# Optimization experiments

Measured on AMD Instinct MI355X. Metric: run time of the kernel, lower is better.

Reference implementation:

```python
import jax, jax.numpy as jnp
import numpy as np

B, S, H, KVH, D, MD = 4, 4096, 2, 1, 2, 5  # batch, seq, heads, kv heads, head_dim, model_dim
EPS, SCALE = 1e-6, 16.0


def _rmsnorm(t):
    # RMSNormNoWeight with scale=16.0 over last dim
    var = jnp.mean(t * t, axis=-1, keepdims=True)
    return SCALE * t * jax.lax.rsqrt(var + EPS)


def _rope(t, cos, sin):
    # t: (B, S, h, D); cos/sin: (S, D//2). Complex multiply on interleaved pairs.
    tr, ti = t[..., 0::2], t[..., 1::2]
    c = cos[None, :, None, :]
    s = sin[None, :, None, :]
    out_r = tr * c - ti * s
    out_i = tr * s + ti * c
    return jnp.stack([out_r, out_i], axis=-1).reshape(t.shape)


def setup_inputs() -> dict:
    key = jax.random.key(0)
    ks = jax.random.split(key, 9)
    return {
        "x": jax.random.normal(ks[0], (B, S, MD), jnp.float32),
        "freqs": jax.random.normal(ks[1], (S, D // 2), jnp.float32),
        "shared_qk_v": jax.random.normal(ks[2], (MD,), jnp.float32),
        "shared_v_v": jax.random.normal(ks[3], (MD,), jnp.float32),
        "shared_o_v": jax.random.normal(ks[4], (H * D,), jnp.float32),
        "shared_vproj_u": jax.random.normal(ks[5], (KVH * D,), jnp.float32),
        "q_u": jax.random.normal(ks[6], (H * D,), jnp.float32),
        "k_u": jax.random.normal(ks[7], (KVH * D,), jnp.float32),
        "o_u": jax.random.normal(ks[8], (MD,), jnp.float32),
    }


def reference(x, freqs, shared_qk_v, shared_v_v, shared_o_v, shared_vproj_u, q_u, k_u, o_u):
    b, s = x.shape[0], x.shape[1]
    # rank-1 projections: (x . v) outer u
    s_qk = jnp.sum(x * shared_qk_v, axis=-1, keepdims=True)  # (B,S,1) shared by q and k
    q = (s_qk * q_u).reshape(b, s, H, D)
    k = (s_qk * k_u).reshape(b, s, KVH, D)
    s_v = jnp.sum(x * shared_v_v, axis=-1, keepdims=True)
    v = (s_v * shared_vproj_u).reshape(b, s, KVH, D)
    # qk-norm + rotary
    q = _rmsnorm(q)
    k = _rmsnorm(k)
    cos, sin = jnp.cos(freqs), jnp.sin(freqs)
    q = _rope(q, cos, sin)
    k = _rope(k, cos, sin)
    # (B,h,S,D)
    q = q.transpose(0, 2, 1, 3)
    k = k.transpose(0, 2, 1, 3)
    v = v.transpose(0, 2, 1, 3)
    # GQA repeat kv heads
    k = jnp.repeat(k, H // KVH, axis=1)
    v = jnp.repeat(v, H // KVH, axis=1)
    scores = jnp.einsum('bhqd,bhkd->bhqk', q, k) / jnp.sqrt(jnp.float32(D))
    probs = jax.nn.softmax(scores, axis=-1)
    out = jnp.einsum('bhqk,bhkd->bhqd', probs, v)
    out = out.transpose(0, 2, 1, 3).reshape(b, s, H * D)
    # rank-1 output projection
    s_o = jnp.sum(out * shared_o_v, axis=-1, keepdims=True)
    return s_o * o_u  # (B,S,MODEL_DIM)
```

## Files before the change

### kernel.cpp

```cpp
#include <hip/hip_runtime.h>
#include <math.h>


#define BQ 4
#define SQ 4096
#define MDQ 5
#define EPSQ 1e-6f
#define SCALEQ 16.0f
#define L2E 1.4426950408889634f
#define ISQ2 0.70710678118654752f

__device__ __forceinline__ float fast_exp2(float x) {
#if __has_builtin(__builtin_amdgcn_exp2f)
    return __builtin_amdgcn_exp2f(x);
#else
    return __expf(x * 0.6931471805599453f);
#endif
}

__global__ __launch_bounds__(256)
void ca_prep(const float* __restrict__ x, const float* __restrict__ freqs,
             const float* __restrict__ qk_v, const float* __restrict__ v_v,
             const float* __restrict__ k_u, float4* __restrict__ pqc)
{
    const int idx = blockIdx.x * 256 + threadIdx.x;
    const int j   = idx & (SQ - 1);

    const float w0 = k_u[0], w1 = k_u[1];
    const float mk = 0.5f * (w0 * w0 + w1 * w1);

    const float qk0 = qk_v[0], qk1 = qk_v[1], qk2 = qk_v[2], qk3 = qk_v[3], qk4 = qk_v[4];
    const float vv0 = v_v[0],  vv1 = v_v[1],  vv2 = v_v[2],  vv3 = v_v[3],  vv4 = v_v[4];

    const float* xr = x + (size_t)idx * MDQ;
    const float x0 = xr[0], x1 = xr[1], x2 = xr[2], x3 = xr[3], x4 = xr[4];
    const float a  = x0*qk0 + x1*qk1 + x2*qk2 + x3*qk3 + x4*qk4;
    const float sv = x0*vv0 + x1*vv1 + x2*vv2 + x3*vv3 + x4*vv4;

    float sj, cj;
    __sincosf(freqs[j], &sj, &cj);
    const float mu = SCALEQ * a * rsqrtf(a * a * mk + EPSQ);
    pqc[idx] = make_float4(mu * cj, mu * sj, sv, 0.0f);
}

#define BLOCK 256
#define ROWS 16
#define SPLIT 16
#define JSUB (SQ / SPLIT)
#define TILES (SQ / ROWS)

__global__ __launch_bounds__(BLOCK)
void ca_main(const float* __restrict__ x,
             const float* __restrict__ freqs,
             const float* __restrict__ qk_v,
             const float* __restrict__ o_v,
             const float* __restrict__ vproj_u,
             const float* __restrict__ q_u,
             const float* __restrict__ k_u,
             const float* __restrict__ o_u,
             const float4* __restrict__ pqc,
             float* __restrict__ out)
{
    __shared__ float4 sRed[ROWS][SPLIT];

    const int tid  = threadIdx.x;
    const int bx   = blockIdx.x;
    const int b    = bx / TILES;
    const int tile = bx % TILES;
    const int row  = tid & (ROWS - 1);
    const int sp   = tid / ROWS;
    const int i    = tile * ROWS + row;

    const float w0 = k_u[0], w1 = k_u[1];
    const float mk  = 0.5f * (w0 * w0 + w1 * w1);
    const float Mmu = SCALEQ * rsqrtf(mk);

    const float qk0 = qk_v[0], qk1 = qk_v[1], qk2 = qk_v[2], qk3 = qk_v[3], qk4 = qk_v[4];
    const float u00 = q_u[0], u01 = q_u[1], u10 = q_u[2], u11 = q_u[3];
    const float m0 = 0.5f * (u00 * u00 + u01 * u01);
    const float m1 = 0.5f * (u10 * u10 + u11 * u11);
    const float A0 = u00 * w0 + u01 * w1, B0 = u01 * w0 - u00 * w1;
    const float A1 = u10 * w0 + u11 * w1, B1 = u11 * w0 - u10 * w1;

    const float* xi = x + (size_t)(b * SQ + i) * MDQ;
    const float ai = xi[0]*qk0 + xi[1]*qk1 + xi[2]*qk2 + xi[3]*qk3 + xi[4]*qk4;
    float si, ci;
    __sincosf(freqs[i], &si, &ci);
    const float lam0 = SCALEQ * ai * rsqrtf(ai * ai * m0 + EPSQ);
    const float lam1 = SCALEQ * ai * rsqrtf(ai * ai * m1 + EPSQ);

    const float alr0 = lam0 * (A0 * ci - B0 * si) * ISQ2;
    const float ber0 = lam0 * (A0 * si + B0 * ci) * ISQ2;
    const float alr1 = lam1 * (A1 * ci - B1 * si) * ISQ2;
    const float ber1 = lam1 * (A1 * si + B1 * ci) * ISQ2;
    const float r0 = sqrtf(alr0 * alr0 + ber0 * ber0);
    const float r1 = sqrtf(alr1 * alr1 + ber1 * ber1);

    const float al0 = alr0 * L2E, be0 = ber0 * L2E, C0 = -r0 * Mmu * L2E;
    const float al1 = alr1 * L2E, be1 = ber1 * L2E, C1 = -r1 * Mmu * L2E;

    const float4* __restrict__ p = pqc + (size_t)b * SQ + sp * JSUB;
    float l0 = 0.f, n0 = 0.f, l1 = 0.f, n1 = 0.f;
#pragma unroll 8
    for (int jj = 0; jj < JSUB; ++jj) {
        const float4 v = p[jj];
        const float s0 = fmaf(al0, v.x, fmaf(be0, v.y, C0));
        const float s1 = fmaf(al1, v.x, fmaf(be1, v.y, C1));
        const float e0 = fast_exp2(s0);
        const float e1 = fast_exp2(s1);
        l0 += e0; n0 = fmaf(e0, v.z, n0);
        l1 += e1; n1 = fmaf(e1, v.z, n1);
    }

    sRed[row][sp] = make_float4(l0, n0, l1, n1);
    __syncthreads();

    if (tid < ROWS) {
        float L0 = 0.f, N0 = 0.f, L1 = 0.f, N1 = 0.f;
#pragma unroll
        for (int s = 0; s < SPLIT; ++s) {
            const float4 t = sRed[tid][s];
            L0 += t.x; N0 += t.y; L1 += t.z; N1 += t.w;
        }
        L0 = fmaxf(L0, 1e-30f);
        L1 = fmaxf(L1, 1e-30f);
        const float W0 = N0 / L0, W1 = N1 / L1;

        const float p0 = vproj_u[0], p1 = vproj_u[1];
        const float d0 = p0 * o_v[0] + p1 * o_v[1];
        const float d1 = p0 * o_v[2] + p1 * o_v[3];
        const float so = W0 * d0 + W1 * d1;

        const int ig = tile * ROWS + tid;
        float* orow = out + (size_t)(b * SQ + ig) * MDQ;
        orow[0] = so * o_u[0];
        orow[1] = so * o_u[1];
        orow[2] = so * o_u[2];
        orow[3] = so * o_u[3];
        orow[4] = so * o_u[4];
    }
}

#define FROWS 32
#define FSPLIT 8
#define FJSUB (SQ / FSPLIT)
#define FTILES (SQ / FROWS)

__global__ __launch_bounds__(256)
void ca_fallback(const float* __restrict__ x,
                 const float* __restrict__ freqs,
                 const float* __restrict__ qk_v,
                 const float* __restrict__ v_v,
                 const float* __restrict__ o_v,
                 const float* __restrict__ vproj_u,
                 const float* __restrict__ q_u,
                 const float* __restrict__ k_u,
                 const float* __restrict__ o_u,
                 float* __restrict__ out)
{
    __shared__ float2 sPQ[SQ];
    __shared__ float  sCv[SQ];
    __shared__ float4 sRed[FROWS][FSPLIT];

    const int tid  = threadIdx.x;
    const int b    = blockIdx.x / FTILES;
    const int tile = blockIdx.x % FTILES;

    const float w0 = k_u[0], w1 = k_u[1];
    const float mk  = 0.5f * (w0 * w0 + w1 * w1);
    const float Mmu = SCALEQ * rsqrtf(mk);

    const float qk0 = qk_v[0], qk1 = qk_v[1], qk2 = qk_v[2], qk3 = qk_v[3], qk4 = qk_v[4];
    const float vv0 = v_v[0],  vv1 = v_v[1],  vv2 = v_v[2],  vv3 = v_v[3],  vv4 = v_v[4];

    for (int k = 0; k < SQ / 256; ++k) {
        const int j = tid + k * 256;
        const float* xr = x + (size_t)(b * SQ + j) * MDQ;
        const float x0 = xr[0], x1 = xr[1], x2 = xr[2], x3 = xr[3], x4 = xr[4];
        const float a  = x0*qk0 + x1*qk1 + x2*qk2 + x3*qk3 + x4*qk4;
        const float sv = x0*vv0 + x1*vv1 + x2*vv2 + x3*vv3 + x4*vv4;
        float sj, cj;
        __sincosf(freqs[j], &sj, &cj);
        const float mu = SCALEQ * a * rsqrtf(a * a * mk + EPSQ);
        sPQ[j] = make_float2(mu * cj, mu * sj);
        sCv[j] = sv;
    }

    const int row = tid & (FROWS - 1);
    const int sp  = tid / FROWS;
    const int i   = tile * FROWS + row;

    const float u00 = q_u[0], u01 = q_u[1], u10 = q_u[2], u11 = q_u[3];
    const float m0 = 0.5f * (u00 * u00 + u01 * u01);
    const float m1 = 0.5f * (u10 * u10 + u11 * u11);
    const float A0 = u00 * w0 + u01 * w1, B0 = u01 * w0 - u00 * w1;
    const float A1 = u10 * w0 + u11 * w1, B1 = u11 * w0 - u10 * w1;

    const float* xi = x + (size_t)(b * SQ + i) * MDQ;
    const float ai = xi[0]*qk0 + xi[1]*qk1 + xi[2]*qk2 + xi[3]*qk3 + xi[4]*qk4;
    float si, ci;
    __sincosf(freqs[i], &si, &ci);
    const float lam0 = SCALEQ * ai * rsqrtf(ai * ai * m0 + EPSQ);
    const float lam1 = SCALEQ * ai * rsqrtf(ai * ai * m1 + EPSQ);
    const float alr0 = lam0 * (A0 * ci - B0 * si) * ISQ2;
    const float ber0 = lam0 * (A0 * si + B0 * ci) * ISQ2;
    const float alr1 = lam1 * (A1 * ci - B1 * si) * ISQ2;
    const float ber1 = lam1 * (A1 * si + B1 * ci) * ISQ2;
    const float r0 = sqrtf(alr0 * alr0 + ber0 * ber0);
    const float r1 = sqrtf(alr1 * alr1 + ber1 * ber1);
    const float al0 = alr0 * L2E, be0 = ber0 * L2E, C0 = -r0 * Mmu * L2E;
    const float al1 = alr1 * L2E, be1 = ber1 * L2E, C1 = -r1 * Mmu * L2E;

    __syncthreads();

    const float2* __restrict__ pq  = sPQ + sp * FJSUB;
    const float*  __restrict__ cvp = sCv + sp * FJSUB;
    float l0 = 0.f, n0 = 0.f, l1 = 0.f, n1 = 0.f;
#pragma unroll 8
    for (int jj = 0; jj < FJSUB; ++jj) {
        const float2 v = pq[jj];
        const float cv = cvp[jj];
        const float s0 = fmaf(al0, v.x, fmaf(be0, v.y, C0));
        const float s1 = fmaf(al1, v.x, fmaf(be1, v.y, C1));
        const float e0 = fast_exp2(s0);
        const float e1 = fast_exp2(s1);
        l0 += e0; n0 = fmaf(e0, cv, n0);
        l1 += e1; n1 = fmaf(e1, cv, n1);
    }

    sRed[row][sp] = make_float4(l0, n0, l1, n1);
    __syncthreads();

    if (tid < FROWS) {
        float L0 = 0.f, N0 = 0.f, L1 = 0.f, N1 = 0.f;
#pragma unroll
        for (int s = 0; s < FSPLIT; ++s) {
            const float4 t = sRed[tid][s];
            L0 += t.x; N0 += t.y; L1 += t.z; N1 += t.w;
        }
        L0 = fmaxf(L0, 1e-30f);
        L1 = fmaxf(L1, 1e-30f);
        const float W0 = N0 / L0, W1 = N1 / L1;
        const float p0 = vproj_u[0], p1 = vproj_u[1];
        const float d0 = p0 * o_v[0] + p1 * o_v[1];
        const float d1 = p0 * o_v[2] + p1 * o_v[3];
        const float so = W0 * d0 + W1 * d1;

        const int ig = tile * FROWS + tid;
        float* orow = out + (size_t)(b * SQ + ig) * MDQ;
        orow[0] = so * o_u[0];
        orow[1] = so * o_u[1];
        orow[2] = so * o_u[2];
        orow[3] = so * o_u[3];
        orow[4] = so * o_u[4];
    }
}

extern "C" void kernel_launch(void* const* d_in, const int* in_sizes, int n_in,
                              void* d_out, int out_size, void* d_ws, size_t ws_size,
                              hipStream_t stream) {
    (void)in_sizes; (void)n_in; (void)out_size;
    const float* x       = (const float*)d_in[0];
    const float* freqs   = (const float*)d_in[1];
    const float* qk_v    = (const float*)d_in[2];
    const float* v_v     = (const float*)d_in[3];
    const float* o_v     = (const float*)d_in[4];
    const float* vproj_u = (const float*)d_in[5];
    const float* q_u     = (const float*)d_in[6];
    const float* k_u     = (const float*)d_in[7];
    const float* o_u     = (const float*)d_in[8];
    float* out = (float*)d_out;

    const size_t pqc_bytes = (size_t)BQ * SQ * sizeof(float4);
    if (ws_size >= pqc_bytes) {
        float4* pqc = (float4*)d_ws;
        hipLaunchKernelGGL(ca_prep, dim3(BQ * SQ / 256), dim3(256), 0, stream,
                           x, freqs, qk_v, v_v, k_u, pqc);
        hipLaunchKernelGGL(ca_main, dim3(BQ * TILES), dim3(BLOCK), 0, stream,
                           x, freqs, qk_v, o_v, vproj_u, q_u, k_u, o_u, pqc, out);
    } else {
        hipLaunchKernelGGL(ca_fallback, dim3(BQ * FTILES), dim3(256), 0, stream,
                           x, freqs, qk_v, v_v, o_v, vproj_u, q_u, k_u, o_u, out);
    }
}
```

Before: 107.7 us.

## Compute multiple query rows per thread and reduce splits with wave shuffles

Each thread now handles four query rows against a strided slice of keys, so every loaded pqc float4 is reused across four rows instead of one. The key split becomes 64 lanes of one wavefront, so the LDS reduction and __syncthreads are replaced by xor-shuffle reductions inside the wave. Coalesced strided loads replace the contiguous per-thread chunks. In exchange, register pressure rises with the four-row accumulator arrays, and the shuffle reduction of 16 values over six steps adds some overhead.

```diff
diff --git a/kernel.cpp b/kernel.cpp
--- a/kernel.cpp
+++ b/kernel.cpp
@@ -44,10 +44,12 @@
 }
 
 #define BLOCK 256
-#define ROWS 16
-#define SPLIT 16
-#define JSUB (SQ / SPLIT)
-#define TILES (SQ / ROWS)
+#define SPLIT 64
+#define RSETS 4
+#define RPT 4
+#define ROWSB (RSETS * RPT)
+#define JITER (SQ / SPLIT)
+#define TILES (SQ / ROWSB)
 
 __global__ __launch_bounds__(BLOCK)
 void ca_main(const float* __restrict__ x,
@@ -61,15 +63,13 @@
              const float4* __restrict__ pqc,
              float* __restrict__ out)
 {
-    __shared__ float4 sRed[ROWS][SPLIT];
-
-    const int tid  = threadIdx.x;
-    const int bx   = blockIdx.x;
-    const int b    = bx / TILES;
+    const int tid = threadIdx.x;
+    const int sp  = tid & 63;
+    const int rs  = tid >> 6;
+    const int bx  = blockIdx.x;
+    const int b   = bx / TILES;
     const int tile = bx % TILES;
-    const int row  = tid & (ROWS - 1);
-    const int sp   = tid / ROWS;
-    const int i    = tile * ROWS + row;
+    const int i0  = tile * ROWSB + rs * RPT;
 
     const float w0 = k_u[0], w1 = k_u[1];
     const float mk  = 0.5f * (w0 * w0 + w1 * w1);
@@ -82,57 +82,68 @@
     const float A0 = u00 * w0 + u01 * w1, B0 = u01 * w0 - u00 * w1;
     const float A1 = u10 * w0 + u11 * w1, B1 = u11 * w0 - u10 * w1;
 
-    const float* xi = x + (size_t)(b * SQ + i) * MDQ;
-    const float ai = xi[0]*qk0 + xi[1]*qk1 + xi[2]*qk2 + xi[3]*qk3 + xi[4]*qk4;
-    float si, ci;
-    __sincosf(freqs[i], &si, &ci);
-    const float lam0 = SCALEQ * ai * rsqrtf(ai * ai * m0 + EPSQ);
-    const float lam1 = SCALEQ * ai * rsqrtf(ai * ai * m1 + EPSQ);
-
-    const float alr0 = lam0 * (A0 * ci - B0 * si) * ISQ2;
-    const float ber0 = lam0 * (A0 * si + B0 * ci) * ISQ2;
-    const float alr1 = lam1 * (A1 * ci - B1 * si) * ISQ2;
-    const float ber1 = lam1 * (A1 * si + B1 * ci) * ISQ2;
-    const float r0 = sqrtf(alr0 * alr0 + ber0 * ber0);
-    const float r1 = sqrtf(alr1 * alr1 + ber1 * ber1);
-
-    const float al0 = alr0 * L2E, be0 = ber0 * L2E, C0 = -r0 * Mmu * L2E;
-    const float al1 = alr1 * L2E, be1 = ber1 * L2E, C1 = -r1 * Mmu * L2E;
-
-    const float4* __restrict__ p = pqc + (size_t)b * SQ + sp * JSUB;
-    float l0 = 0.f, n0 = 0.f, l1 = 0.f, n1 = 0.f;
-#pragma unroll 8
-    for (int jj = 0; jj < JSUB; ++jj) {
-        const float4 v = p[jj];
-        const float s0 = fmaf(al0, v.x, fmaf(be0, v.y, C0));
-        const float s1 = fmaf(al1, v.x, fmaf(be1, v.y, C1));
-        const float e0 = fast_exp2(s0);
-        const float e1 = fast_exp2(s1);
-        l0 += e0; n0 = fmaf(e0, v.z, n0);
-        l1 += e1; n1 = fmaf(e1, v.z, n1);
-    }
-
-    sRed[row][sp] = make_float4(l0, n0, l1, n1);
-    __syncthreads();
-
-    if (tid < ROWS) {
-        float L0 = 0.f, N0 = 0.f, L1 = 0.f, N1 = 0.f;
-#pragma unroll
-        for (int s = 0; s < SPLIT; ++s) {
-            const float4 t = sRed[tid][s];
-            L0 += t.x; N0 += t.y; L1 += t.z; N1 += t.w;
+    float al0[RPT], be0[RPT], C0[RPT], al1[RPT], be1[RPT], C1[RPT];
+#pragma unroll
+    for (int k = 0; k < RPT; ++k) {
+        const int i = i0 + k;
+        const float* xi = x + (size_t)(b * SQ + i) * MDQ;
+        const float ai = xi[0]*qk0 + xi[1]*qk1 + xi[2]*qk2 + xi[3]*qk3 + xi[4]*qk4;
+        float si, ci;
+        __sincosf(freqs[i], &si, &ci);
+        const float lam0 = SCALEQ * ai * rsqrtf(ai * ai * m0 + EPSQ);
+        const float lam1 = SCALEQ * ai * rsqrtf(ai * ai * m1 + EPSQ);
+        const float a0 = lam0 * (A0 * ci - B0 * si) * ISQ2;
+        const float b0_ = lam0 * (A0 * si + B0 * ci) * ISQ2;
+        const float a1 = lam1 * (A1 * ci - B1 * si) * ISQ2;
+        const float b1_ = lam1 * (A1 * si + B1 * ci) * ISQ2;
+        const float r0 = sqrtf(a0 * a0 + b0_ * b0_);
+        const float r1 = sqrtf(a1 * a1 + b1_ * b1_);
+        al0[k] = a0 * L2E;  be0[k] = b0_ * L2E;  C0[k] = -r0 * Mmu * L2E;
+        al1[k] = a1 * L2E;  be1[k] = b1_ * L2E;  C1[k] = -r1 * Mmu * L2E;
+    }
+
+    const float4* __restrict__ p = pqc + (size_t)b * SQ + sp;
+    float l0[RPT], n0[RPT], l1[RPT], n1[RPT];
+#pragma unroll
+    for (int k = 0; k < RPT; ++k) { l0[k] = 0.f; n0[k] = 0.f; l1[k] = 0.f; n1[k] = 0.f; }
+
+#pragma unroll 4
+    for (int jj = 0; jj < JITER; ++jj) {
+        const float4 v = p[(size_t)jj * 64];
+#pragma unroll
+        for (int k = 0; k < RPT; ++k) {
+            const float s0 = fmaf(al0[k], v.x, fmaf(be0[k], v.y, C0[k]));
+            const float s1 = fmaf(al1[k], v.x, fmaf(be1[k], v.y, C1[k]));
+            const float e0 = fast_exp2(s0);
+            const float e1 = fast_exp2(s1);
+            l0[k] += e0;  n0[k] = fmaf(e0, v.z, n0[k]);
+            l1[k] += e1;  n1[k] = fmaf(e1, v.z, n1[k]);
         }
-        L0 = fmaxf(L0, 1e-30f);
-        L1 = fmaxf(L1, 1e-30f);
-        const float W0 = N0 / L0, W1 = N1 / L1;
+    }
+
+#pragma unroll
+    for (int m = 1; m < 64; m <<= 1) {
+#pragma unroll
+        for (int k = 0; k < RPT; ++k) {
+            l0[k] += __shfl_xor(l0[k], m, 64);
+            n0[k] += __shfl_xor(n0[k], m, 64);
+            l1[k] += __shfl_xor(l1[k], m, 64);
+            n1[k] += __shfl_xor(n1[k], m, 64);
+        }
+    }
+
+    if (sp < RPT) {
+        const int k = sp;
+        const float L0 = fmaxf(l0[k], 1e-30f);
+        const float L1 = fmaxf(l1[k], 1e-30f);
+        const float W0 = n0[k] / L0, W1 = n1[k] / L1;
 
         const float p0 = vproj_u[0], p1 = vproj_u[1];
         const float d0 = p0 * o_v[0] + p1 * o_v[1];
         const float d1 = p0 * o_v[2] + p1 * o_v[3];
         const float so = W0 * d0 + W1 * d1;
 
-        const int ig = tile * ROWS + tid;
-        float* orow = out + (size_t)(b * SQ + ig) * MDQ;
+        float* orow = out + (size_t)(b * SQ + i0 + k) * MDQ;
         orow[0] = so * o_u[0];
         orow[1] = so * o_u[1];
         orow[2] = so * o_u[2];
```

After: 96.87 us. 1.11x faster.
